# Performance work log

Measured on AMD Instinct MI355X. Metric: run time of the kernel, lower is better.

The kernel has to match this reference:

```python
import jax, jax.numpy as jnp
import numpy as np

# Multi-scale schedule for (T,H,W)=(1,16,16) from get_latent2scale_schedule
SCHEDULE = [(1, 1, 1), (1, 2, 2), (1, 3, 3), (1, 4, 4), (1, 5, 5),
            (1, 6, 6), (1, 8, 8), (1, 10, 10), (1, 13, 13), (1, 16, 16)]

N_EMBED = 196560  # Leech lattice kissing number
EMBED_DIM = 24


def _resize(x, thw):
    # x: [B, D, T, H, W] -> [B, D, t, h, w] (trilinear/bilinear interpolation)
    b, d = x.shape[:2]
    return jax.image.resize(x, (b, d) + tuple(thw), method='bilinear')


def _quantize(r, codebook):
    """SphericalVectorQuantizer with predefined (pre-normalized) codebook.
    r: [B, D, t, h, w].  d = -z @ codebook^T; argmin(d) == argmax(sim)."""
    b, d = r.shape[0], r.shape[1]
    spatial = r.shape[2:]
    zf = jnp.moveaxis(r, 1, -1).reshape(-1, d)            # [N, D] tokens
    sim = zf @ codebook.T                                  # [N, K] cosine similarity
    idx = jnp.argmax(jax.lax.stop_gradient(sim), axis=1)   # argmin of -sim
    zq = codebook[idx]                                     # gather [N, D]
    zq = zq / jnp.linalg.norm(zq, axis=-1, keepdims=True)  # F.normalize (no-op if unit)
    zq = zf + jax.lax.stop_gradient(zq - zf)               # straight-through estimator
    zq = jnp.moveaxis(zq.reshape((b,) + spatial + (d,)), -1, 1)
    return zq, idx


def setup_inputs() -> dict:
    key = jax.random.key(0)
    k1, k2 = jax.random.split(key)
    z = jax.random.normal(k1, (2, 24, 1, 16, 16), jnp.float32)
    cb = jax.random.normal(k2, (N_EMBED, EMBED_DIM), jnp.float32)
    cb = cb / jnp.linalg.norm(cb, axis=-1, keepdims=True)  # normalized Leech codebook
    return {"z": z, "codebook": cb}


def reference(z, codebook):
    # Multi-scale residual quantization (Algorithm 1, RQ-style):
    # downsample residual -> spherical VQ (STE) -> upsample -> accumulate/subtract.
    B, D, T, H, W = z.shape
    residual = z
    z_hat = jnp.zeros_like(z)
    all_idx = []
    for thw in SCHEDULE:
        r_down = _resize(residual, thw)
        zq, idx = _quantize(r_down, codebook)
        zq_up = _resize(zq, (T, H, W))
        z_hat = z_hat + zq_up
        residual = residual - jax.lax.stop_gradient(zq_up)  # residual detach (default)
        all_idx.append(idx)
    indices = jnp.concatenate(all_idx)  # [B * sum(t*h*w)] int codes
    return z_hat, indices
```

## Files before the change

### kernel.cpp

```cpp
#include <hip/hip_runtime.h>
#include <stdint.h>

#define KCB 196560
#define DIM 24
#define BB  2
#define ZEL 12288
#define NRB 384
#define RBS 512

typedef __attribute__((ext_vector_type(8)))  __bf16 bf16x8;
typedef __attribute__((ext_vector_type(16))) float  f32x16;

__device__ __forceinline__ unsigned long long pack_key(float sim, int idx) {
  unsigned u = __float_as_uint(sim);
  u = (u & 0x80000000u) ? ~u : (u | 0x80000000u);
  return ((unsigned long long)u << 32) | (unsigned)(~(unsigned)idx);
}

__global__ __launch_bounds__(256) void init_kernel(const float* __restrict__ z,
    float* __restrict__ residual, float* __restrict__ out, int outTotal) {
  int e = blockIdx.x * 256 + threadIdx.x;
  if (e < ZEL) residual[e] = z[e];
  if (e < outTotal) out[e] = 0.0f;
}

__global__ __launch_bounds__(256) void down_kernel(const float* __restrict__ residual,
    float* __restrict__ rdown, unsigned long long* __restrict__ best, int t, int n) {
  int gid = blockIdx.x * 256 + threadIdx.x;
  if (gid < BB * n) best[gid] = 0ull;
  int total = BB * DIM * n;
  if (gid >= total) return;
  int sp = gid % n;
  int d  = (gid / n) % DIM;
  int b  = gid / (n * DIM);
  int oh = sp / t, ow = sp - oh * t;
  float inv_scale = 16.0f / (float)t;
  float ks = inv_scale;
  float sf_h = ((float)oh + 0.5f) * inv_scale - 0.5f;
  float sf_w = ((float)ow + 0.5f) * inv_scale - 0.5f;
  float wh[16], ww[16];
  float sh = 0.f, sw = 0.f;
#pragma unroll
  for (int i = 0; i < 16; ++i) {
    float vh = fmaxf(0.f, 1.f - fabsf(sf_h - (float)i) / ks);
    wh[i] = vh; sh += vh;
    float vw = fmaxf(0.f, 1.f - fabsf(sf_w - (float)i) / ks);
    ww[i] = vw; sw += vw;
  }
#pragma unroll
  for (int i = 0; i < 16; ++i) { wh[i] /= sh; ww[i] /= sw; }
  const float* resb = residual + (b * DIM + d) * 256;
  float acc = 0.f;
  for (int ih = 0; ih < 16; ++ih) {
    float ra = 0.f;
#pragma unroll
    for (int iw = 0; iw < 16; ++iw) ra = fmaf(ww[iw], resb[ih * 16 + iw], ra);
    acc = fmaf(wh[ih], ra, acc);
  }
  rdown[(b * n + sp) * DIM + d] = acc;
}

__device__ __forceinline__ void load8(const float* p, float* xs) {
  float4 a = *(const float4*)p;
  float4 b = *(const float4*)(p + 4);
  xs[0]=a.x; xs[1]=a.y; xs[2]=a.z; xs[3]=a.w;
  xs[4]=b.x; xs[5]=b.y; xs[6]=b.z; xs[7]=b.w;
}

__device__ __forceinline__ void cvt_hi_lo(const float* xs, uint4& hw, uint4& lw) {
  unsigned h[8], l[8];
#pragma unroll
  for (int j = 0; j < 8; ++j) {
    unsigned b = __float_as_uint(xs[j]);
    h[j] = b >> 16;
    float hif = __uint_as_float(b & 0xffff0000u);
    float lof = xs[j] - hif;
    l[j] = __float_as_uint(lof) >> 16;
  }
  hw = make_uint4(h[0] | (h[1] << 16), h[2] | (h[3] << 16),
                  h[4] | (h[5] << 16), h[6] | (h[7] << 16));
  lw = make_uint4(l[0] | (l[1] << 16), l[2] | (l[3] << 16),
                  l[4] | (l[5] << 16), l[6] | (l[7] << 16));
}

__global__ __launch_bounds__(256) void score_kernel(const float* __restrict__ rdown,
    const float* __restrict__ cb, float* __restrict__ blockmax, int T) {
  const int bx = blockIdx.x;
  const int rb = bx % NRB, tb = bx / NRB;
  const int tid = threadIdx.x, lane = tid & 63, wv = tid >> 6;
  const int col = lane & 31, g = lane >> 5;
  const int tbase = tb * 128;
  const int ntt = min(4, (T - tbase + 31) >> 5);

  bf16x8 bhi[4][2], blo[4][2];
#pragma unroll
  for (int tt = 0; tt < 4; ++tt) {
    int token = tbase + tt * 32 + col;
    bool tv = (tt < ntt) && (token < T);
    const float* tr = rdown + token * DIM;
    uint4 h0 = make_uint4(0,0,0,0), l0 = h0, h1 = h0, l1 = h0;
    if (tv) { float xs[8]; load8(tr + g * 8, xs); cvt_hi_lo(xs, h0, l0); }
    if (tv && g == 0) { float xs[8]; load8(tr + 16, xs); cvt_hi_lo(xs, h1, l1); }
    bhi[tt][0] = __builtin_bit_cast(bf16x8, h0);
    blo[tt][0] = __builtin_bit_cast(bf16x8, l0);
    bhi[tt][1] = __builtin_bit_cast(bf16x8, h1);
    blo[tt][1] = __builtin_bit_cast(bf16x8, l1);
  }

  const f32x16 fzero = {};
  float runmax[4] = {-3.402823466e38f, -3.402823466e38f, -3.402823466e38f, -3.402823466e38f};
  const int rbase = rb * RBS + wv * 128;

#pragma unroll
  for (int rt = 0; rt < 4; ++rt) {
    int tilebase = rbase + rt * 32;
    if (tilebase >= KCB) continue;
    int row = tilebase + col;
    bool rv = row < KCB;
    const float* cr = cb + (size_t)row * DIM;
    uint4 h0 = make_uint4(0,0,0,0), l0 = h0, h1 = h0, l1 = h0;
    if (rv) { float xs[8]; load8(cr + g * 8, xs); cvt_hi_lo(xs, h0, l0); }
    if (rv && g == 0) { float xs[8]; load8(cr + 16, xs); cvt_hi_lo(xs, h1, l1); }
    bf16x8 ah0 = __builtin_bit_cast(bf16x8, h0);
    bf16x8 al0 = __builtin_bit_cast(bf16x8, l0);
    bf16x8 ah1 = __builtin_bit_cast(bf16x8, h1);
    bf16x8 al1 = __builtin_bit_cast(bf16x8, l1);
    int limit = KCB - tilebase;
    bool full = limit >= 32;
#pragma unroll
    for (int tt = 0; tt < 4; ++tt) {
      if (tt >= ntt) continue;
      f32x16 acc = __builtin_amdgcn_mfma_f32_32x32x16_bf16(ah0, bhi[tt][0], fzero, 0, 0, 0);
      acc = __builtin_amdgcn_mfma_f32_32x32x16_bf16(ah1, bhi[tt][1], acc, 0, 0, 0);
      acc = __builtin_amdgcn_mfma_f32_32x32x16_bf16(al0, bhi[tt][0], acc, 0, 0, 0);
      acc = __builtin_amdgcn_mfma_f32_32x32x16_bf16(al1, bhi[tt][1], acc, 0, 0, 0);
      acc = __builtin_amdgcn_mfma_f32_32x32x16_bf16(ah0, blo[tt][0], acc, 0, 0, 0);
      acc = __builtin_amdgcn_mfma_f32_32x32x16_bf16(ah1, blo[tt][1], acc, 0, 0, 0);
      float m;
      if (full) {
        float m01 = fmaxf(acc[0], acc[1]),  m23 = fmaxf(acc[2], acc[3]);
        float m45 = fmaxf(acc[4], acc[5]),  m67 = fmaxf(acc[6], acc[7]);
        float m89 = fmaxf(acc[8], acc[9]),  mab = fmaxf(acc[10], acc[11]);
        float mcd = fmaxf(acc[12], acc[13]), mef = fmaxf(acc[14], acc[15]);
        m = fmaxf(fmaxf(fmaxf(m01, m23), fmaxf(m45, m67)),
                  fmaxf(fmaxf(m89, mab), fmaxf(mcd, mef)));
      } else {
        m = -3.402823466e38f;
#pragma unroll
        for (int r = 0; r < 16; ++r) {
          int rowid = (r & 3) + 8 * (r >> 2) + 4 * g;
          if (rowid < limit) m = fmaxf(m, acc[r]);
        }
      }
      runmax[tt] = fmaxf(runmax[tt], m);
    }
  }

  __shared__ float lmax[4][4][32];
#pragma unroll
  for (int tt = 0; tt < 4; ++tt) {
    float v = fmaxf(runmax[tt], __shfl_xor(runmax[tt], 32));
    if (lane < 32) lmax[wv][tt][col] = v;
  }
  __syncthreads();
  if (tid < 128) {
    int tt = tid >> 5, c = tid & 31;
    if (tt < ntt) {
      float m = fmaxf(fmaxf(lmax[0][tt][c], lmax[1][tt][c]),
                      fmaxf(lmax[2][tt][c], lmax[3][tt][c]));
      int token = tbase + tt * 32 + c;
      if (token < T) blockmax[token * NRB + rb] = m;
    }
  }
}

__global__ __launch_bounds__(256) void finalize_kernel(const float* __restrict__ cb,
    const float* __restrict__ rdown, const float* __restrict__ blockmax,
    unsigned long long* __restrict__ best, int T) {
  int tid = threadIdx.x, lane = tid & 63, wv = tid >> 6;
  int tok = blockIdx.x * 4 + wv;
  if (tok >= T) return;

  float x = (lane < DIM) ? rdown[tok * DIM + lane] : 0.f;
  float av[DIM];
#pragma unroll
  for (int k = 0; k < DIM; ++k)
    av[k] = __uint_as_float(__builtin_amdgcn_readlane(__float_as_uint(x), k));
  float ss = 0.f;
#pragma unroll
  for (int k = 0; k < DIM; ++k) ss = fmaf(av[k], av[k], ss);
  float eps = 1e-3f * sqrtf(ss) + 1e-30f;

  const float* bmrow = blockmax + (size_t)tok * NRB;
  float bv[6];
#pragma unroll
  for (int i = 0; i < 6; ++i) bv[i] = bmrow[lane + 64 * i];
  float M = fmaxf(fmaxf(fmaxf(bv[0], bv[1]), fmaxf(bv[2], bv[3])), fmaxf(bv[4], bv[5]));
#pragma unroll
  for (int d = 32; d; d >>= 1) M = fmaxf(M, __shfl_xor(M, d));
  float thr = M - eps;

  unsigned long long bk = 0ull;
#pragma unroll
  for (int i = 0; i < 6; ++i) {
    unsigned long long mask = __ballot(bv[i] >= thr);
    while (mask) {
      int l = __ffsll((unsigned long long)mask) - 1;
      mask &= mask - 1;
      int rowb = (l + 64 * i) * RBS;
      for (int r8 = 0; r8 < 8; ++r8) {
        int row = rowb + r8 * 64 + lane;
        if (row < KCB) {
          const float* cv = cb + (size_t)row * DIM;
          float acc = 0.f;
#pragma unroll
          for (int k = 0; k < DIM; ++k) acc = fmaf(av[k], cv[k], acc);
          unsigned long long key = pack_key(acc, row);
          if (key > bk) bk = key;
        }
      }
    }
  }
#pragma unroll
  for (int d = 32; d; d >>= 1) {
    unsigned long long o = __shfl_xor(bk, d);
    if (o > bk) bk = o;
  }
  if (lane == 0) best[tok] = bk;
}

template<int TSZ>
__global__ __launch_bounds__(256) void update_kernel(const float* __restrict__ cb,
    const unsigned long long* __restrict__ best, float* __restrict__ residual,
    float* __restrict__ out, int idxBase) {
  constexpr int N = TSZ * TSZ;
  constexpr int T = BB * N;
  __shared__ float zq[T * DIM];
  int tid = threadIdx.x;
  for (int slot = tid; slot < T; slot += 256) {
    unsigned long long key = best[slot];
    int idx = (int)(~(unsigned)key);
    const float* cv = cb + (long long)idx * DIM;
    float v[DIM]; float ss = 0.f;
#pragma unroll
    for (int k = 0; k < DIM; ++k) { v[k] = cv[k]; ss = fmaf(v[k], v[k], ss); }
    float nrm = sqrtf(ss);
#pragma unroll
    for (int k = 0; k < DIM; ++k) zq[slot * DIM + k] = v[k] / nrm;
    if (blockIdx.x == 0) out[idxBase + slot] = (float)idx;
  }
  __syncthreads();
  int e = blockIdx.x * 256 + tid;
  int w = e & 15, h = (e >> 4) & 15;
  int d = (e >> 8) % DIM;
  int b = e / (DIM * 256);
  float inv_scale = (float)TSZ / 16.0f;
  float sf_h = ((float)h + 0.5f) * inv_scale - 0.5f;
  float sf_w = ((float)w + 0.5f) * inv_scale - 0.5f;
  float wh[TSZ], ww[TSZ];
  float sh = 0.f, sw = 0.f;
#pragma unroll
  for (int j = 0; j < TSZ; ++j) {
    float vh = fmaxf(0.f, 1.f - fabsf(sf_h - (float)j));
    wh[j] = vh; sh += vh;
    float vw = fmaxf(0.f, 1.f - fabsf(sf_w - (float)j));
    ww[j] = vw; sw += vw;
  }
#pragma unroll
  for (int j = 0; j < TSZ; ++j) { wh[j] /= sh; ww[j] /= sw; }
  const float* zb = zq + (b * N) * DIM + d;
  float acc = 0.f;
#pragma unroll
  for (int th = 0; th < TSZ; ++th) {
    float ra = 0.f;
#pragma unroll
    for (int tw = 0; tw < TSZ; ++tw) ra = fmaf(ww[tw], zb[(th * TSZ + tw) * DIM], ra);
    acc = fmaf(wh[th], ra, acc);
  }
  out[e] += acc;
  residual[e] -= acc;
}

extern "C" void kernel_launch(void* const* d_in, const int* in_sizes, int n_in,
                              void* d_out, int out_size, void* d_ws, size_t ws_size,
                              hipStream_t stream) {
  const float* z  = (const float*)d_in[0];
  const float* cb = (const float*)d_in[1];
  float* out = (float*)d_out;
  float* residual = (float*)d_ws;
  float* rdown = residual + ZEL;
  float* blockmax = rdown + ZEL;
  unsigned long long* best =
      (unsigned long long*)(blockmax + 512 * NRB);

  static const int TS[10] = {1, 2, 3, 4, 5, 6, 8, 10, 13, 16};

  init_kernel<<<(out_size + 255) / 256, 256, 0, stream>>>(z, residual, out, out_size);

  int prefix = 0;
  for (int s = 0; s < 10; ++s) {
    int t = TS[s], n = t * t, T = BB * n;
    int dtotal = BB * DIM * n;
    down_kernel<<<(dtotal + 255) / 256, 256, 0, stream>>>(residual, rdown, best, t, n);

    int ntb = (T + 127) >> 7;
    score_kernel<<<NRB * ntb, 256, 0, stream>>>(rdown, cb, blockmax, T);
    finalize_kernel<<<(T + 3) / 4, 256, 0, stream>>>(cb, rdown, blockmax, best, T);

    int idxBase = ZEL + BB * prefix;
    switch (t) {
      case 1:  update_kernel<1><<<48, 256, 0, stream>>>(cb, best, residual, out, idxBase); break;
      case 2:  update_kernel<2><<<48, 256, 0, stream>>>(cb, best, residual, out, idxBase); break;
      case 3:  update_kernel<3><<<48, 256, 0, stream>>>(cb, best, residual, out, idxBase); break;
      case 4:  update_kernel<4><<<48, 256, 0, stream>>>(cb, best, residual, out, idxBase); break;
      case 5:  update_kernel<5><<<48, 256, 0, stream>>>(cb, best, residual, out, idxBase); break;
      case 6:  update_kernel<6><<<48, 256, 0, stream>>>(cb, best, residual, out, idxBase); break;
      case 8:  update_kernel<8><<<48, 256, 0, stream>>>(cb, best, residual, out, idxBase); break;
      case 10: update_kernel<10><<<48, 256, 0, stream>>>(cb, best, residual, out, idxBase); break;
      case 13: update_kernel<13><<<48, 256, 0, stream>>>(cb, best, residual, out, idxBase); break;
      case 16: update_kernel<16><<<48, 256, 0, stream>>>(cb, best, residual, out, idxBase); break;
    }
    prefix += n;
  }
}
```

Before: 370.2 us.

## Precompute bf16 codebook once, pre-pack token hi/lo, drop codebook low term

A new prep kernel converts the fp32 codebook to bf16 high halves once per call, and the score kernel reads these 16-bit rows instead of loading and splitting fp32 rows on every scale. The downsample kernel is restructured to produce four channels per thread and also writes the bf16 hi/lo token splits, so the score kernel no longer converts tokens. The codebook low-part MFMAs are dropped, going from six to four per tile. This lowers codebook bandwidth and conversion ALU work per scale, but scores become less exact. To compensate, the finalize rescoring tolerance is widened from 1e-3 to 0.02 of the token norm, which can send more candidate blocks through the exact fp32 rescoring pass.

```diff
diff --git a/kernel.cpp b/kernel.cpp
--- a/kernel.cpp
+++ b/kernel.cpp
@@ -24,15 +24,27 @@
   if (e < outTotal) out[e] = 0.0f;
 }
 
-__global__ __launch_bounds__(256) void down_kernel(const float* __restrict__ residual,
-    float* __restrict__ rdown, unsigned long long* __restrict__ best, int t, int n) {
-  int gid = blockIdx.x * 256 + threadIdx.x;
-  if (gid < BB * n) best[gid] = 0ull;
-  int total = BB * DIM * n;
-  if (gid >= total) return;
-  int sp = gid % n;
-  int d  = (gid / n) % DIM;
-  int b  = gid / (n * DIM);
+__global__ __launch_bounds__(256) void cbprep_kernel(const float* __restrict__ cb,
+    ushort* __restrict__ ch) {
+  int j = blockIdx.x * 256 + threadIdx.x;
+  if (j >= KCB * 6) return;
+  int row = j / 6, q = j - row * 6;
+  float4 v = *(const float4*)(cb + (size_t)row * 24 + q * 4);
+  unsigned b0 = __float_as_uint(v.x) >> 16;
+  unsigned b1 = __float_as_uint(v.y) >> 16;
+  unsigned b2 = __float_as_uint(v.z) >> 16;
+  unsigned b3 = __float_as_uint(v.w) >> 16;
+  *(uint2*)(ch + (size_t)row * 24 + q * 4) = make_uint2(b0 | (b1 << 16), b2 | (b3 << 16));
+}
+
+__global__ __launch_bounds__(256) void down_pack_kernel(const float* __restrict__ residual,
+    float* __restrict__ rdown, ushort* __restrict__ th, ushort* __restrict__ tl,
+    int t, int n) {
+  int j = blockIdx.x * 256 + threadIdx.x;
+  int T = BB * n;
+  if (j >= 6 * T) return;
+  int token = j / 6, q = j - token * 6;
+  int b = token / n, sp = token - b * n;
   int oh = sp / t, ow = sp - oh * t;
   float inv_scale = 16.0f / (float)t;
   float ks = inv_scale;
@@ -49,62 +61,60 @@
   }
 #pragma unroll
   for (int i = 0; i < 16; ++i) { wh[i] /= sh; ww[i] /= sw; }
-  const float* resb = residual + (b * DIM + d) * 256;
-  float acc = 0.f;
-  for (int ih = 0; ih < 16; ++ih) {
-    float ra = 0.f;
-#pragma unroll
-    for (int iw = 0; iw < 16; ++iw) ra = fmaf(ww[iw], resb[ih * 16 + iw], ra);
-    acc = fmaf(wh[ih], ra, acc);
-  }
-  rdown[(b * n + sp) * DIM + d] = acc;
-}
-
-__device__ __forceinline__ void load8(const float* p, float* xs) {
-  float4 a = *(const float4*)p;
-  float4 b = *(const float4*)(p + 4);
-  xs[0]=a.x; xs[1]=a.y; xs[2]=a.z; xs[3]=a.w;
-  xs[4]=b.x; xs[5]=b.y; xs[6]=b.z; xs[7]=b.w;
-}
-
-__device__ __forceinline__ void cvt_hi_lo(const float* xs, uint4& hw, uint4& lw) {
-  unsigned h[8], l[8];
-#pragma unroll
-  for (int j = 0; j < 8; ++j) {
-    unsigned b = __float_as_uint(xs[j]);
-    h[j] = b >> 16;
-    float hif = __uint_as_float(b & 0xffff0000u);
-    float lof = xs[j] - hif;
-    l[j] = __float_as_uint(lof) >> 16;
-  }
-  hw = make_uint4(h[0] | (h[1] << 16), h[2] | (h[3] << 16),
-                  h[4] | (h[5] << 16), h[6] | (h[7] << 16));
-  lw = make_uint4(l[0] | (l[1] << 16), l[2] | (l[3] << 16),
-                  l[4] | (l[5] << 16), l[6] | (l[7] << 16));
-}
-
-__global__ __launch_bounds__(256) void score_kernel(const float* __restrict__ rdown,
-    const float* __restrict__ cb, float* __restrict__ blockmax, int T) {
+  float acc4[4];
+#pragma unroll
+  for (int dd = 0; dd < 4; ++dd) {
+    int d = q * 4 + dd;
+    const float* resb = residual + (b * DIM + d) * 256;
+    float acc = 0.f;
+    for (int ih = 0; ih < 16; ++ih) {
+      float ra = 0.f;
+#pragma unroll
+      for (int iw = 0; iw < 16; ++iw) ra = fmaf(ww[iw], resb[ih * 16 + iw], ra);
+      acc = fmaf(wh[ih], ra, acc);
+    }
+    acc4[dd] = acc;
+  }
+  *(float4*)(rdown + (size_t)token * 24 + q * 4) =
+      make_float4(acc4[0], acc4[1], acc4[2], acc4[3]);
+  unsigned h[4], l[4];
+#pragma unroll
+  for (int dd = 0; dd < 4; ++dd) {
+    unsigned bits = __float_as_uint(acc4[dd]);
+    h[dd] = bits >> 16;
+    float hif = __uint_as_float(bits & 0xffff0000u);
+    l[dd] = __float_as_uint(acc4[dd] - hif) >> 16;
+  }
+  *(uint2*)(th + (size_t)token * 24 + q * 4) = make_uint2(h[0] | (h[1] << 16), h[2] | (h[3] << 16));
+  *(uint2*)(tl + (size_t)token * 24 + q * 4) = make_uint2(l[0] | (l[1] << 16), l[2] | (l[3] << 16));
+}
+
+__global__ __launch_bounds__(256) void score_kernel(const ushort* __restrict__ ch,
+    const ushort* __restrict__ th, const ushort* __restrict__ tl,
+    float* __restrict__ blockmax, int T) {
   const int bx = blockIdx.x;
   const int rb = bx % NRB, tb = bx / NRB;
   const int tid = threadIdx.x, lane = tid & 63, wv = tid >> 6;
   const int col = lane & 31, g = lane >> 5;
   const int tbase = tb * 128;
   const int ntt = min(4, (T - tbase + 31) >> 5);
-
-  bf16x8 bhi[4][2], blo[4][2];
+  const uint4 z4 = make_uint4(0, 0, 0, 0);
+
+  bf16x8 bh[4][2], bl[4][2];
 #pragma unroll
   for (int tt = 0; tt < 4; ++tt) {
     int token = tbase + tt * 32 + col;
     bool tv = (tt < ntt) && (token < T);
-    const float* tr = rdown + token * DIM;
-    uint4 h0 = make_uint4(0,0,0,0), l0 = h0, h1 = h0, l1 = h0;
-    if (tv) { float xs[8]; load8(tr + g * 8, xs); cvt_hi_lo(xs, h0, l0); }
-    if (tv && g == 0) { float xs[8]; load8(tr + 16, xs); cvt_hi_lo(xs, h1, l1); }
-    bhi[tt][0] = __builtin_bit_cast(bf16x8, h0);
-    blo[tt][0] = __builtin_bit_cast(bf16x8, l0);
-    bhi[tt][1] = __builtin_bit_cast(bf16x8, h1);
-    blo[tt][1] = __builtin_bit_cast(bf16x8, l1);
+    const ushort* tr = th + (size_t)token * 24;
+    const ushort* sr = tl + (size_t)token * 24;
+    uint4 h0 = tv ? *(const uint4*)(tr + g * 8) : z4;
+    uint4 h1 = (tv && g == 0) ? *(const uint4*)(tr + 16) : z4;
+    uint4 l0 = tv ? *(const uint4*)(sr + g * 8) : z4;
+    uint4 l1 = (tv && g == 0) ? *(const uint4*)(sr + 16) : z4;
+    bh[tt][0] = __builtin_bit_cast(bf16x8, h0);
+    bh[tt][1] = __builtin_bit_cast(bf16x8, h1);
+    bl[tt][0] = __builtin_bit_cast(bf16x8, l0);
+    bl[tt][1] = __builtin_bit_cast(bf16x8, l1);
   }
 
   const f32x16 fzero = {};
@@ -117,25 +127,20 @@
     if (tilebase >= KCB) continue;
     int row = tilebase + col;
     bool rv = row < KCB;
-    const float* cr = cb + (size_t)row * DIM;
-    uint4 h0 = make_uint4(0,0,0,0), l0 = h0, h1 = h0, l1 = h0;
-    if (rv) { float xs[8]; load8(cr + g * 8, xs); cvt_hi_lo(xs, h0, l0); }
-    if (rv && g == 0) { float xs[8]; load8(cr + 16, xs); cvt_hi_lo(xs, h1, l1); }
-    bf16x8 ah0 = __builtin_bit_cast(bf16x8, h0);
-    bf16x8 al0 = __builtin_bit_cast(bf16x8, l0);
-    bf16x8 ah1 = __builtin_bit_cast(bf16x8, h1);
-    bf16x8 al1 = __builtin_bit_cast(bf16x8, l1);
+    const ushort* cr = ch + (size_t)row * 24;
+    uint4 a0 = rv ? *(const uint4*)(cr + g * 8) : z4;
+    uint4 a1 = (rv && g == 0) ? *(const uint4*)(cr + 16) : z4;
+    bf16x8 ah0 = __builtin_bit_cast(bf16x8, a0);
+    bf16x8 ah1 = __builtin_bit_cast(bf16x8, a1);
     int limit = KCB - tilebase;
     bool full = limit >= 32;
 #pragma unroll
     for (int tt = 0; tt < 4; ++tt) {
       if (tt >= ntt) continue;
-      f32x16 acc = __builtin_amdgcn_mfma_f32_32x32x16_bf16(ah0, bhi[tt][0], fzero, 0, 0, 0);
-      acc = __builtin_amdgcn_mfma_f32_32x32x16_bf16(ah1, bhi[tt][1], acc, 0, 0, 0);
-      acc = __builtin_amdgcn_mfma_f32_32x32x16_bf16(al0, bhi[tt][0], acc, 0, 0, 0);
-      acc = __builtin_amdgcn_mfma_f32_32x32x16_bf16(al1, bhi[tt][1], acc, 0, 0, 0);
-      acc = __builtin_amdgcn_mfma_f32_32x32x16_bf16(ah0, blo[tt][0], acc, 0, 0, 0);
-      acc = __builtin_amdgcn_mfma_f32_32x32x16_bf16(ah1, blo[tt][1], acc, 0, 0, 0);
+      f32x16 acc = __builtin_amdgcn_mfma_f32_32x32x16_bf16(ah0, bh[tt][0], fzero, 0, 0, 0);
+      acc = __builtin_amdgcn_mfma_f32_32x32x16_bf16(ah1, bh[tt][1], acc, 0, 0, 0);
+      acc = __builtin_amdgcn_mfma_f32_32x32x16_bf16(ah0, bl[tt][0], acc, 0, 0, 0);
+      acc = __builtin_amdgcn_mfma_f32_32x32x16_bf16(ah1, bl[tt][1], acc, 0, 0, 0);
       float m;
       if (full) {
         float m01 = fmaxf(acc[0], acc[1]),  m23 = fmaxf(acc[2], acc[3]);
@@ -189,7 +194,7 @@
   float ss = 0.f;
 #pragma unroll
   for (int k = 0; k < DIM; ++k) ss = fmaf(av[k], av[k], ss);
-  float eps = 1e-3f * sqrtf(ss) + 1e-30f;
+  float eps = 0.02f * sqrtf(ss) + 1e-30f;
 
   const float* bmrow = blockmax + (size_t)tok * NRB;
   float bv[6];
@@ -292,19 +297,22 @@
   float* blockmax = rdown + ZEL;
   unsigned long long* best =
       (unsigned long long*)(blockmax + 512 * NRB);
+  ushort* th = (ushort*)(best + 512);
+  ushort* tl = th + 512 * 24;
+  ushort* ch = tl + 512 * 24;
 
   static const int TS[10] = {1, 2, 3, 4, 5, 6, 8, 10, 13, 16};
 
   init_kernel<<<(out_size + 255) / 256, 256, 0, stream>>>(z, residual, out, out_size);
+  cbprep_kernel<<<(KCB * 6 + 255) / 256, 256, 0, stream>>>(cb, ch);
 
   int prefix = 0;
   for (int s = 0; s < 10; ++s) {
     int t = TS[s], n = t * t, T = BB * n;
-    int dtotal = BB * DIM * n;
-    down_kernel<<<(dtotal + 255) / 256, 256, 0, stream>>>(residual, rdown, best, t, n);
+    down_pack_kernel<<<(6 * T + 255) / 256, 256, 0, stream>>>(residual, rdown, th, tl, t, n);
 
     int ntb = (T + 127) >> 7;
-    score_kernel<<<NRB * ntb, 256, 0, stream>>>(rdown, cb, blockmax, T);
+    score_kernel<<<NRB * ntb, 256, 0, stream>>>(ch, th, tl, blockmax, T);
     finalize_kernel<<<(T + 3) / 4, 256, 0, stream>>>(cb, rdown, blockmax, best, T);
 
     int idxBase = ZEL + BB * prefix;
```

Measured after the change: 703.4 us. 90.0% more time.
